# Kernel optimization log

Measured on AMD Instinct MI355X. Metric: run time of the kernel, lower is better.

The kernel has to match this reference:

```python
import math
import jax, jax.numpy as jnp
import numpy as np

HID = 256; NH = 8; DH = 32; DFF = 1024  # int(4.0*256)
N = 10000; E = 160000; NV = 128; NG = 64


def _ln(x, eps=1e-6):
    m = jnp.mean(x, axis=-1, keepdims=True)
    v = jnp.mean((x - m) ** 2, axis=-1, keepdims=True)
    return (x - m) * jax.lax.rsqrt(v + eps)


def _modulate(x, shift, scale):
    return x * (1.0 + scale) + shift


def _swiglu(x, W12, Wout):
    a, b = jnp.split(x @ W12, 2, axis=-1)
    return (jax.nn.silu(a) * b) @ Wout


def _adaln(t, W, b):
    return jnp.split(jax.nn.silu(t) @ W + b, 6, axis=-1)


def setup_inputs() -> dict:
    key = jax.random.key(0)
    ks = jax.random.split(key, 32)
    rn = lambda k, shape, s=1.0: jax.random.normal(k, shape, jnp.float32) * s
    W = 0.02
    return {
        "batch": jnp.sort(jax.random.randint(ks[0], (N,), 0, NG)),
        "x": rn(ks[1], (N, HID)),
        "t_emb_h": rn(ks[2], (N, HID)),
        "edge_attr": rn(ks[3], (E, HID)),
        "edge_index": jax.random.randint(ks[4], (2, E), 0, N),
        "t_emb_e": rn(ks[5], (E, HID)),
        "dist": rn(ks[6], (E, NV)),
        "W_edge_emb": rn(ks[7], (HID + NV, HID), W),
        "b_edge_emb": jnp.zeros((HID,), jnp.float32),
        "W_adaln": rn(ks[8], (HID, 6 * HID), W),
        "b_adaln": jnp.zeros((6 * HID,), jnp.float32),
        "W_adaln_e": rn(ks[9], (HID, 6 * HID), W),
        "b_adaln_e": jnp.zeros((6 * HID,), jnp.float32),
        "W_qkv": rn(ks[10], (HID, 3 * HID), W),
        "W_e0": rn(ks[11], (HID, HID), W),
        "W_e1": rn(ks[12], (HID, HID), W),
        "W_n2e": rn(ks[13], (HID, HID), W),
        "b_n2e": jnp.zeros((HID,), jnp.float32),
        "g_ln": jnp.ones((HID,), jnp.float32),
        "b_ln": jnp.zeros((HID,), jnp.float32),
        "W_ffn12": rn(ks[14], (HID, 2 * DFF), W),
        "W_ffn_out": rn(ks[15], (DFF, HID), W),
        "W_ffne12": rn(ks[16], (HID, 2 * DFF), W),
        "W_ffne_out": rn(ks[17], (DFF, HID), W),
    }


def reference(batch, x, t_emb_h, edge_attr, edge_index, t_emb_e, dist,
              W_edge_emb, b_edge_emb, W_adaln, b_adaln, W_adaln_e, b_adaln_e,
              W_qkv, W_e0, W_e1, W_n2e, b_n2e, g_ln, b_ln,
              W_ffn12, W_ffn_out, W_ffne12, W_ffne_out):
    src, tgt = edge_index[0], edge_index[1]
    n = x.shape[0]
    h_in_node = x
    h_in_edge = edge_attr

    shift_msa, scale_msa, gate_msa, shift_mlp, scale_mlp, gate_mlp = _adaln(t_emb_h, W_adaln, b_adaln)
    e_shift_msa, e_scale_msa, e_gate_msa, e_shift_mlp, e_scale_mlp, e_gate_mlp = _adaln(t_emb_e, W_adaln_e, b_adaln_e)

    edge_attr_e = jnp.concatenate([edge_attr, dist], axis=-1) @ W_edge_emb + b_edge_emb
    x_mod = _modulate(_ln(x), shift_msa, scale_msa)
    prev_edge_attr = edge_attr_e
    e_mod = _modulate(_ln(edge_attr_e), e_shift_msa, e_scale_msa)

    qkv = x_mod @ W_qkv                         # N x 3H
    Q, K, V = jnp.split(qkv, 3, axis=-1)
    Q = Q.reshape(-1, NH, DH)
    K = K.reshape(-1, NH, DH)
    V = V.reshape(-1, NH, DH)

    query_i = Q[src]                            # E x NH x DH
    key_j = K[tgt]
    value_j = V[tgt]
    edge_attn = jax.nn.gelu(e_mod @ W_e0, approximate=True).reshape(-1, NH, DH)

    alpha = jnp.sum(query_i * key_j * edge_attn, axis=-1) / math.sqrt(DH)  # E x NH
    # segment softmax over edges grouped by target node
    amax = jax.ops.segment_max(alpha, tgt, num_segments=n)                 # N x NH
    exp_a = jnp.exp(alpha - amax[tgt])
    denom = jax.ops.segment_sum(exp_a, tgt, num_segments=n)
    alpha = exp_a / denom[tgt]

    msg = value_j * (e_mod @ W_e1).reshape(-1, NH, DH) * alpha[..., None]
    out = jax.ops.segment_sum(msg.reshape(-1, NH * DH), tgt, num_segments=n)  # N x H

    h_node = out
    h_edge = (h_node[src] + h_node[tgt]) @ W_n2e + b_n2e

    h_node = h_in_node + gate_msa * h_node
    h_node = _modulate(_ln(h_node) * g_ln + b_ln, shift_mlp, scale_mlp)
    h_out = h_node + gate_mlp * _swiglu(h_node, W_ffn12, W_ffn_out)

    h_edge = h_in_edge + e_gate_msa * h_edge
    h_edge = _modulate(_ln(h_edge), e_shift_mlp, e_scale_mlp)
    h_edge_out = prev_edge_attr + h_edge + e_gate_mlp * _swiglu(h_edge, W_ffne12, W_ffne_out)
    return (h_out, h_edge_out)
```

## Files before the change

### kernel.cpp

```cpp
#include <hip/hip_runtime.h>

#define HID 256

typedef unsigned short u16;
typedef __attribute__((ext_vector_type(8))) short bf16x8;
typedef __attribute__((ext_vector_type(4))) float f32x4;

__device__ __forceinline__ float siluf(float x) { return x / (1.f + __expf(-x)); }
__device__ __forceinline__ float geluf(float x) {
    return x / (1.f + __expf(-(1.59576912f * x + 0.07135481f * x * x * x)));
}
__device__ __forceinline__ u16 f2b(float x) {
    unsigned u = __float_as_uint(x);
    unsigned r = u + 0x7FFFu + ((u >> 16) & 1u);
    return (u16)(r >> 16);
}
__device__ __forceinline__ float b2f(u16 h) {
    return __uint_as_float(((unsigned)h) << 16);
}
__device__ __forceinline__ void gload16(const u16* g, u16* l) {
    __builtin_amdgcn_global_load_lds(
        (const __attribute__((address_space(1))) unsigned int*)g,
        (__attribute__((address_space(3))) unsigned int*)l, 16, 0, 0);
}
__device__ __forceinline__ int imin(int a, int b) { return a < b ? a : b; }

__global__ __launch_bounds__(256) void gemm_mfma(
    const u16* __restrict__ A, int lda,
    const u16* __restrict__ Bt, int ldb,
    void* __restrict__ Cv, int ldc,
    int M, int N, int K,
    const float* __restrict__ bias, int act, int obf16)
{
    __shared__ u16 lds[8192];

    const int tid  = threadIdx.x;
    const int lane = tid & 63;
    const int wave = tid >> 6;
    const int row0 = blockIdx.y * 64;
    const int col0 = blockIdx.x * 128;
    const int wm   = (wave >> 1) * 32;
    const int wn   = (wave & 1) * 64;

    f32x4 acc[2][4];
#pragma unroll
    for (int i = 0; i < 2; ++i)
#pragma unroll
        for (int j = 0; j < 4; ++j) acc[i][j] = (f32x4)0.0f;

    const int kc = (lane & 3) * 8;
    const int rr  = wave * 16 + (lane >> 2);
    const int rb1 = (wave + 4) * 16 + (lane >> 2);
    const u16* pa  = A + (size_t)imin(row0 + rr, M - 1) * lda + kc;
    const u16* pb0 = Bt + (size_t)(col0 + rr) * ldb + kc;
    const u16* pb1 = Bt + (size_t)(col0 + rb1) * ldb + kc;
    u16* la  = &lds[wave * 512];
    u16* lb0 = &lds[2048 + wave * 512];
    u16* lb1 = &lds[2048 + (wave + 4) * 512];

    const int kb = (lane >> 4) * 8;
    const int fr = lane & 15;

    for (int k0 = 0; k0 < K; k0 += 32) {
        gload16(pa + k0, la);
        gload16(pb0 + k0, lb0);
        gload16(pb1 + k0, lb1);
        __syncthreads();

        bf16x8 af[2], bfm[4];
#pragma unroll
        for (int i = 0; i < 2; ++i)
            af[i] = *(const bf16x8*)&lds[(wm + i * 16 + fr) * 32 + kb];
#pragma unroll
        for (int j = 0; j < 4; ++j)
            bfm[j] = *(const bf16x8*)&lds[2048 + (wn + j * 16 + fr) * 32 + kb];
#pragma unroll
        for (int i = 0; i < 2; ++i)
#pragma unroll
            for (int j = 0; j < 4; ++j)
                acc[i][j] = __builtin_amdgcn_mfma_f32_16x16x32_bf16(af[i], bfm[j], acc[i][j], 0, 0, 0);
        __syncthreads();
    }

    const int qr = (lane >> 4) * 4;
    if (obf16) {
#pragma unroll
        for (int i = 0; i < 2; ++i)
#pragma unroll
            for (int r = 0; r < 4; ++r)
#pragma unroll
                for (int j = 0; j < 4; ++j) {
                    int lcol = wn + j * 16 + fr;
                    int gcol = col0 + lcol;
                    float v = acc[i][j][r];
                    if (bias) v += bias[gcol];
                    if (act == 2) v = geluf(v);
                    else if (act == 1) v = siluf(v);
                    else if (act == 4 && gcol < 256) v = geluf(v);
                    lds[(wm + i * 16 + qr + r) * 128 + lcol] = f2b(v);
                }
        __syncthreads();
        int row = tid >> 2, cc0 = (tid & 3) * 32;
        int grow = row0 + row;
        if (grow < M) {
            uint4* dst = (uint4*)((u16*)Cv + (size_t)grow * ldc + col0 + cc0);
            const uint4* sp = (const uint4*)&lds[row * 128 + cc0];
            dst[0] = sp[0]; dst[1] = sp[1]; dst[2] = sp[2]; dst[3] = sp[3];
        }
    } else {
        float* Cf = (float*)Cv;
#pragma unroll
        for (int i = 0; i < 2; ++i)
#pragma unroll
            for (int r = 0; r < 4; ++r) {
                int grow = row0 + wm + i * 16 + qr + r;
                if (grow >= M) continue;
#pragma unroll
                for (int j = 0; j < 4; ++j) {
                    int gcol = col0 + wn + j * 16 + fr;
                    float v = acc[i][j][r];
                    if (bias) v += bias[gcol];
                    if (act == 2) v = geluf(v);
                    else if (act == 1) v = siluf(v);
                    Cf[(size_t)grow * ldc + gcol] = v;
                }
            }
    }
}

__global__ __launch_bounds__(256) void gemm_ffn12(
    const u16* __restrict__ A, const u16* __restrict__ Wt,
    u16* __restrict__ C, int M)
{
    __shared__ u16 sm[6144];
    u16* lsA = sm;
    u16* lsB1 = sm + 2048;
    u16* lsB2 = sm + 4096;

    const int tid  = threadIdx.x;
    const int lane = tid & 63;
    const int wave = tid >> 6;
    const int row0 = blockIdx.y * 64;
    const int col0 = blockIdx.x * 64;
    const int wm   = (wave >> 1) * 32;
    const int wn   = (wave & 1) * 32;

    f32x4 accA[2][2], accB[2][2];
#pragma unroll
    for (int i = 0; i < 2; ++i)
#pragma unroll
        for (int j = 0; j < 2; ++j) { accA[i][j] = (f32x4)0.0f; accB[i][j] = (f32x4)0.0f; }

    const int kc = (lane & 3) * 8;
    const int rr = wave * 16 + (lane >> 2);
    const u16* pa  = A + (size_t)imin(row0 + rr, M - 1) * 256 + kc;
    const u16* pb1 = Wt + (size_t)(col0 + rr) * 256 + kc;
    const u16* pb2 = Wt + (size_t)(1024 + col0 + rr) * 256 + kc;
    u16* la  = &lsA[wave * 512];
    u16* lb1 = &lsB1[wave * 512];
    u16* lb2 = &lsB2[wave * 512];

    const int kb = (lane >> 4) * 8;
    const int fr = lane & 15;

#pragma unroll 1
    for (int k0 = 0; k0 < 256; k0 += 32) {
        gload16(pa + k0, la);
        gload16(pb1 + k0, lb1);
        gload16(pb2 + k0, lb2);
        __syncthreads();

        bf16x8 af[2], b1f[2], b2f_[2];
#pragma unroll
        for (int i = 0; i < 2; ++i)
            af[i] = *(const bf16x8*)&lsA[(wm + i * 16 + fr) * 32 + kb];
#pragma unroll
        for (int j = 0; j < 2; ++j) {
            b1f[j] = *(const bf16x8*)&lsB1[(wn + j * 16 + fr) * 32 + kb];
            b2f_[j] = *(const bf16x8*)&lsB2[(wn + j * 16 + fr) * 32 + kb];
        }
#pragma unroll
        for (int i = 0; i < 2; ++i)
#pragma unroll
            for (int j = 0; j < 2; ++j) {
                accA[i][j] = __builtin_amdgcn_mfma_f32_16x16x32_bf16(af[i], b1f[j], accA[i][j], 0, 0, 0);
                accB[i][j] = __builtin_amdgcn_mfma_f32_16x16x32_bf16(af[i], b2f_[j], accB[i][j], 0, 0, 0);
            }
        __syncthreads();
    }

    const int qr = (lane >> 4) * 4;
#pragma unroll
    for (int i = 0; i < 2; ++i)
#pragma unroll
        for (int r = 0; r < 4; ++r)
#pragma unroll
            for (int j = 0; j < 2; ++j) {
                float a = accA[i][j][r], b = accB[i][j][r];
                sm[(wm + i * 16 + qr + r) * 64 + wn + j * 16 + fr] = f2b(siluf(a) * b);
            }
    __syncthreads();
    int row = tid >> 2, cc0 = (tid & 3) * 16;
    int grow = row0 + row;
    if (grow < M) {
        uint4* dst = (uint4*)(C + (size_t)grow * 1024 + col0 + cc0);
        const uint4* sp = (const uint4*)&sm[row * 64 + cc0];
        dst[0] = sp[0]; dst[1] = sp[1];
    }
}

__global__ __launch_bounds__(256) void gemm_out_final(
    const u16* __restrict__ A, const u16* __restrict__ Bt,
    const float* __restrict__ eae, const u16* __restrict__ h2,
    const u16* __restrict__ gate, int ldg, int goff,
    float* __restrict__ out, int M)
{
    __shared__ u16 lds[6144];

    const int tid  = threadIdx.x;
    const int lane = tid & 63;
    const int wave = tid >> 6;
    const int row0 = blockIdx.y * 64;
    const int col0 = blockIdx.x * 128;
    const int wm   = (wave >> 1) * 32;
    const int wn   = (wave & 1) * 64;

    f32x4 acc[2][4];
#pragma unroll
    for (int i = 0; i < 2; ++i)
#pragma unroll
        for (int j = 0; j < 4; ++j) acc[i][j] = (f32x4)0.0f;

    const int kc = (lane & 3) * 8;
    const int rr = wave * 16 + (lane >> 2);
    const int rb0 = wave * 16 + (lane >> 2), rb1 = (wave + 4) * 16 + (lane >> 2);
    const u16* pa  = A + (size_t)imin(row0 + rr, M - 1) * 1024 + kc;
    const u16* pb0 = Bt + (size_t)(col0 + rb0) * 1024 + kc;
    const u16* pb1 = Bt + (size_t)(col0 + rb1) * 1024 + kc;
    u16* la  = &lds[wave * 512];
    u16* lb0 = &lds[2048 + wave * 512];
    u16* lb1 = &lds[2048 + (wave + 4) * 512];

    const int kb = (lane >> 4) * 8;
    const int fr = lane & 15;

#pragma unroll 1
    for (int k0 = 0; k0 < 1024; k0 += 32) {
        gload16(pa + k0, la);
        gload16(pb0 + k0, lb0);
        gload16(pb1 + k0, lb1);
        __syncthreads();

        bf16x8 af[2], bfm[4];
#pragma unroll
        for (int i = 0; i < 2; ++i)
            af[i] = *(const bf16x8*)&lds[(wm + i * 16 + fr) * 32 + kb];
#pragma unroll
        for (int j = 0; j < 4; ++j)
            bfm[j] = *(const bf16x8*)&lds[2048 + (wn + j * 16 + fr) * 32 + kb];
#pragma unroll
        for (int i = 0; i < 2; ++i)
#pragma unroll
            for (int j = 0; j < 4; ++j)
                acc[i][j] = __builtin_amdgcn_mfma_f32_16x16x32_bf16(af[i], bfm[j], acc[i][j], 0, 0, 0);
        __syncthreads();
    }

    const int qr = (lane >> 4) * 4;
#pragma unroll
    for (int i = 0; i < 2; ++i)
#pragma unroll
        for (int r = 0; r < 4; ++r) {
            int grow = row0 + wm + i * 16 + qr + r;
            if (grow >= M) continue;
#pragma unroll
            for (int j = 0; j < 4; ++j) {
                int gcol = col0 + wn + j * 16 + fr;
                size_t idx = (size_t)grow * 256 + gcol;
                float v = acc[i][j][r] * b2f(gate[(size_t)grow * ldg + goff + gcol]) + b2f(h2[idx]);
                if (eae) v += eae[idx];
                out[idx] = v;
            }
        }
}

__global__ __launch_bounds__(256) void k_wconv(
    const float* __restrict__ W, u16* __restrict__ Wt, int K, int N)
{
    int i = blockIdx.x * 256 + threadIdx.x;
    if (i >= K * N) return;
    int n = i / K, k = i - n * K;
    Wt[i] = f2b(W[(size_t)k * N + n]);
}

__global__ __launch_bounds__(256) void k_silu_b16(
    const float* __restrict__ src, u16* __restrict__ dst, long long n4)
{
    long long i = (long long)blockIdx.x * 256 + threadIdx.x;
    if (i >= n4) return;
    float4 v = ((const float4*)src)[i];
    ushort4 o;
    o.x = f2b(siluf(v.x)); o.y = f2b(siluf(v.y)); o.z = f2b(siluf(v.z)); o.w = f2b(siluf(v.w));
    ((ushort4*)dst)[i] = o;
}

__global__ __launch_bounds__(256) void k_pack_ed(
    const float* __restrict__ ea_, const float* __restrict__ dist,
    u16* __restrict__ out, long long cnt4)
{
    long long i = (long long)blockIdx.x * 256 + threadIdx.x;
    if (i >= cnt4) return;
    long long r = i / 96;
    int c4 = (int)(i - r * 96) * 4;
    float4 v = (c4 < 256) ? *(const float4*)(ea_ + r * 256 + c4)
                          : *(const float4*)(dist + r * 128 + (c4 - 256));
    ushort4 o;
    o.x = f2b(v.x); o.y = f2b(v.y); o.z = f2b(v.z); o.w = f2b(v.w);
    *(ushort4*)(out + r * 384 + c4) = o;
}

__global__ __launch_bounds__(256) void k_ln_mod_b16(
    const float* __restrict__ X, u16* __restrict__ Y, int M,
    const u16* __restrict__ ssb, int ldss, int shoff, int scoff)
{
    int row = (blockIdx.x << 2) + (threadIdx.x >> 6);
    if (row >= M) return;
    int lane = threadIdx.x & 63;
    const float* xr = X + (size_t)row * HID + lane * 4;
    float x0 = xr[0], x1 = xr[1], x2 = xr[2], x3 = xr[3];
    float s = x0 + x1 + x2 + x3;
    float q = x0 * x0 + x1 * x1 + x2 * x2 + x3 * x3;
#pragma unroll
    for (int o = 32; o; o >>= 1) { s += __shfl_xor(s, o, 64); q += __shfl_xor(q, o, 64); }
    float m = s * (1.f / HID);
    float r = rsqrtf(q * (1.f / HID) - m * m + 1e-6f);
    const u16* sp = ssb + (size_t)row * ldss;
    ushort4 sh = *(const ushort4*)(sp + shoff + lane * 4);
    ushort4 sc = *(const ushort4*)(sp + scoff + lane * 4);
    ushort4 o;
    o.x = f2b((x0 - m) * r * (1.f + b2f(sc.x)) + b2f(sh.x));
    o.y = f2b((x1 - m) * r * (1.f + b2f(sc.y)) + b2f(sh.y));
    o.z = f2b((x2 - m) * r * (1.f + b2f(sc.z)) + b2f(sh.z));
    o.w = f2b((x3 - m) * r * (1.f + b2f(sc.w)) + b2f(sh.w));
    ((ushort4*)(Y + (size_t)row * HID))[lane] = o;
}

__global__ __launch_bounds__(256) void k_ln_mod_resid_b16(
    const float* __restrict__ A, const float* __restrict__ Bv, u16* __restrict__ Y, int M,
    const u16* __restrict__ gb, int ldg, int goff,
    const u16* __restrict__ ssb, int ldss, int shoff, int scoff,
    const float* __restrict__ gw, const float* __restrict__ bw)
{
    int row = (blockIdx.x << 2) + (threadIdx.x >> 6);
    if (row >= M) return;
    int lane = threadIdx.x & 63;
    const float* ar = A + (size_t)row * HID + lane * 4;
    const float* br = Bv + (size_t)row * HID + lane * 4;
    ushort4 gp = *(const ushort4*)(gb + (size_t)row * ldg + goff + lane * 4);
    float t0 = ar[0] + b2f(gp.x) * br[0];
    float t1 = ar[1] + b2f(gp.y) * br[1];
    float t2 = ar[2] + b2f(gp.z) * br[2];
    float t3 = ar[3] + b2f(gp.w) * br[3];
    float s = t0 + t1 + t2 + t3;
    float q = t0 * t0 + t1 * t1 + t2 * t2 + t3 * t3;
#pragma unroll
    for (int o = 32; o; o >>= 1) { s += __shfl_xor(s, o, 64); q += __shfl_xor(q, o, 64); }
    float m = s * (1.f / HID);
    float r = rsqrtf(q * (1.f / HID) - m * m + 1e-6f);
    float n0 = (t0 - m) * r, n1 = (t1 - m) * r, n2 = (t2 - m) * r, n3 = (t3 - m) * r;
    if (gw) {
        const float* g4 = gw + lane * 4;
        const float* b4 = bw + lane * 4;
        n0 = n0 * g4[0] + b4[0]; n1 = n1 * g4[1] + b4[1];
        n2 = n2 * g4[2] + b4[2]; n3 = n3 * g4[3] + b4[3];
    }
    const u16* sp = ssb + (size_t)row * ldss;
    ushort4 sh = *(const ushort4*)(sp + shoff + lane * 4);
    ushort4 sc = *(const ushort4*)(sp + scoff + lane * 4);
    ushort4 o;
    o.x = f2b(n0 * (1.f + b2f(sc.x)) + b2f(sh.x));
    o.y = f2b(n1 * (1.f + b2f(sc.y)) + b2f(sh.y));
    o.z = f2b(n2 * (1.f + b2f(sc.z)) + b2f(sh.z));
    o.w = f2b(n3 * (1.f + b2f(sc.w)) + b2f(sh.w));
    ((ushort4*)(Y + (size_t)row * HID))[lane] = o;
}

__global__ __launch_bounds__(256) void attn_alpha_k(
    const u16* __restrict__ qkv, const u16* __restrict__ ea, int lde,
    const int* __restrict__ src, const int* __restrict__ tgt,
    float* __restrict__ alpha)
{
    int e = blockIdx.x;
    int t = threadIdx.x;
    int h = t >> 5, d = t & 31;
    int s = src[e], g = tgt[e];
    float qv = b2f(qkv[(size_t)s * 768 + h * 32 + d]);
    float kv = b2f(qkv[(size_t)g * 768 + 256 + h * 32 + d]);
    float wv = b2f(ea[(size_t)e * lde + t]);
    float v = qv * kv * wv;
#pragma unroll
    for (int o = 16; o; o >>= 1) v += __shfl_xor(v, o, 32);
    if (d == 0) alpha[(size_t)e * 8 + h] = v * 0.17677669529663687f;
}

__global__ __launch_bounds__(256) void k_hist(
    const int* __restrict__ tgt, int* __restrict__ counts, int E)
{
    int i = blockIdx.x * 256 + threadIdx.x;
    if (i < E) atomicAdd(&counts[tgt[i]], 1);
}

__global__ __launch_bounds__(256) void k_scan(
    const int* __restrict__ counts, int* __restrict__ offsets, int Nn)
{
    __shared__ int part[256];
    __shared__ int pref[257];
    int t = threadIdx.x;
    int chunk = (Nn + 255) / 256;
    int lo = t * chunk, hi = imin(lo + chunk, Nn);
    int s = 0;
    for (int i = lo; i < hi; ++i) s += counts[i];
    part[t] = s;
    __syncthreads();
    if (t == 0) {
        int run = 0;
        for (int i = 0; i < 256; ++i) { pref[i] = run; run += part[i]; }
        pref[256] = run;
        offsets[Nn] = run;
    }
    __syncthreads();
    int run = pref[t];
    for (int i = lo; i < hi; ++i) { offsets[i] = run; run += counts[i]; }
}

__global__ __launch_bounds__(256) void k_scatter(
    const int* __restrict__ tgt, int* __restrict__ cursor,
    int* __restrict__ eidlist, int E)
{
    int i = blockIdx.x * 256 + threadIdx.x;
    if (i < E) {
        int pos = atomicAdd(&cursor[tgt[i]], 1);
        eidlist[pos] = i;
    }
}

__global__ __launch_bounds__(256) void k_amax_den(
    const float* __restrict__ alpha, const int* __restrict__ offsets,
    const int* __restrict__ eidlist, float* __restrict__ amaxF,
    float* __restrict__ invden, int NH8)
{
    int i = blockIdx.x * 256 + threadIdx.x;
    if (i >= NH8) return;
    int n = i >> 3, h = i & 7;
    int b = offsets[n], e = offsets[n + 1];
    float m = -1e30f;
    for (int k = b; k < e; ++k) m = fmaxf(m, alpha[(size_t)eidlist[k] * 8 + h]);
    float s = 0.f;
    for (int k = b; k < e; ++k) s += __expf(alpha[(size_t)eidlist[k] * 8 + h] - m);
    amaxF[i] = m;
    invden[i] = (s > 0.f) ? 1.f / s : 0.f;
}

__global__ __launch_bounds__(256) void k_norm(
    float* __restrict__ alpha, const float* __restrict__ amaxF,
    const float* __restrict__ invden, const int* __restrict__ tgt, int EH)
{
    int i = blockIdx.x * 256 + threadIdx.x;
    if (i >= EH) return;
    int e = i >> 3, h = i & 7;
    int g = tgt[e];
    alpha[i] = __expf(alpha[i] - amaxF[(size_t)g * 8 + h]) * invden[(size_t)g * 8 + h];
}

__global__ __launch_bounds__(256) void attn_msg_csr(
    const u16* __restrict__ qkv, const u16* __restrict__ ea1,
    const float* __restrict__ alpha, const int* __restrict__ offsets,
    const int* __restrict__ eidlist, float* __restrict__ hattn)
{
    int n = blockIdx.x;
    int c = threadIdx.x;
    int h = c >> 5;
    int b = offsets[n], e = offsets[n + 1];
    float acc = 0.f;
    for (int k = b; k < e; ++k) {
        int eid = eidlist[k];
        float w = alpha[(size_t)eid * 8 + h];
        acc += b2f(ea1[(size_t)eid * 512 + 256 + c]) * w;
    }
    hattn[(size_t)n * 256 + c] = b2f(qkv[(size_t)n * 768 + 512 + c]) * acc;
}

__global__ __launch_bounds__(256) void k_gsum_b16(
    const float* __restrict__ hattn, const int* __restrict__ src, const int* __restrict__ tgt,
    u16* __restrict__ g, long long cnt4)
{
    long long i = (long long)blockIdx.x * 256 + threadIdx.x;
    if (i >= cnt4) return;
    long long e = i >> 6;
    int c4 = (int)(i & 63) * 4;
    float4 a = *(const float4*)(hattn + (size_t)src[e] * 256 + c4);
    float4 b = *(const float4*)(hattn + (size_t)tgt[e] * 256 + c4);
    ushort4 o;
    o.x = f2b(a.x + b.x); o.y = f2b(a.y + b.y); o.z = f2b(a.z + b.z); o.w = f2b(a.w + b.w);
    ((ushort4*)g)[i] = o;
}

static inline void gemm(hipStream_t st, const u16* A, int lda, const u16* Bt, int ldb,
                        void* C, int ldc, int M, int N, int K,
                        const float* bias, int act, int obf16)
{
    dim3 g(N / 128, (M + 63) / 64);
    hipLaunchKernelGGL(gemm_mfma, g, dim3(256), 0, st, A, lda, Bt, ldb, C, ldc, M, N, K,
                       bias, act, obf16);
}

extern "C" void kernel_launch(void* const* d_in, const int* in_sizes, int n_in,
                              void* d_out, int out_size, void* d_ws, size_t ws_size,
                              hipStream_t stream)
{
    const int Nn = in_sizes[0];
    const int E = in_sizes[3] / HID;

    const float* x        = (const float*)d_in[1];
    const float* t_emb_h  = (const float*)d_in[2];
    const float* edge_attr= (const float*)d_in[3];
    const int*   eidx     = (const int*)d_in[4];
    const float* t_emb_e  = (const float*)d_in[5];
    const float* dist     = (const float*)d_in[6];
    const float* W_ee     = (const float*)d_in[7];
    const float* b_ee     = (const float*)d_in[8];
    const float* W_ad     = (const float*)d_in[9];
    const float* b_ad     = (const float*)d_in[10];
    const float* W_ade    = (const float*)d_in[11];
    const float* b_ade    = (const float*)d_in[12];
    const float* W_qkv    = (const float*)d_in[13];
    const float* W_e0     = (const float*)d_in[14];
    const float* W_e1     = (const float*)d_in[15];
    const float* W_n2e    = (const float*)d_in[16];
    const float* b_n2e    = (const float*)d_in[17];
    const float* g_ln     = (const float*)d_in[18];
    const float* b_ln     = (const float*)d_in[19];
    const float* W_f12    = (const float*)d_in[20];
    const float* W_fout   = (const float*)d_in[21];
    const float* W_fe12   = (const float*)d_in[22];
    const float* W_feout  = (const float*)d_in[23];

    const int* src = eidx;
    const int* tgt = eidx + E;

    float* outN = (float*)d_out;
    float* outE = (float*)d_out + (size_t)Nn * 256;

    char* W = (char*)d_ws;
    size_t off = 0;
    auto alloc = [&](size_t bytes) -> size_t {
        size_t o = off; off += (bytes + 255) & ~(size_t)255; return o;
    };
    float*    alpha = (float*)(W + alloc((size_t)E * 8 * 4));
    float*    amaxF = (float*)(W + alloc((size_t)Nn * 8 * 4));
    float*    invden= (float*)(W + alloc((size_t)Nn * 8 * 4));
    float*    hat   = (float*)(W + alloc((size_t)Nn * 256 * 4));
    int*      offs  = (int*)(W + alloc((size_t)(Nn + 1) * 4));
    int*      cursor= (int*)(W + alloc((size_t)Nn * 4));
    int*      eidl  = (int*)(W + alloc((size_t)E * 4));
    u16*      qkvb  = (u16*)(W + alloc((size_t)Nn * 768 * 2));
    u16*      sth   = (u16*)(W + alloc((size_t)Nn * 256 * 2));
    u16*      steb  = (u16*)(W + alloc((size_t)E * 256 * 2));
    u16*      ea1b  = (u16*)(W + alloc((size_t)E * 512 * 2));
    u16*      adnb  = (u16*)(W + alloc((size_t)Nn * 1536 * 2));
    u16*      xmb   = (u16*)(W + alloc((size_t)Nn * 256 * 2));
    u16*      h2nb  = (u16*)(W + alloc((size_t)Nn * 256 * 2));
    u16*      cnb   = (u16*)(W + alloc((size_t)Nn * 1024 * 2));
    u16* weet   = (u16*)(W + alloc((size_t)256 * 384 * 2));
    u16* wadt   = (u16*)(W + alloc((size_t)1536 * 256 * 2));
    u16* wadet  = (u16*)(W + alloc((size_t)1536 * 256 * 2));
    u16* wqkvt  = (u16*)(W + alloc((size_t)768 * 256 * 2));
    u16* we01t  = (u16*)(W + alloc((size_t)512 * 256 * 2));
    u16* wn2et  = (u16*)(W + alloc((size_t)256 * 256 * 2));
    u16* wf12t  = (u16*)(W + alloc((size_t)2048 * 256 * 2));
    u16* wfoutt = (u16*)(W + alloc((size_t)256 * 1024 * 2));
    u16* wfe12t = (u16*)(W + alloc((size_t)2048 * 256 * 2));
    u16* wfeoutt= (u16*)(W + alloc((size_t)256 * 1024 * 2));

    char* pool = W + off;
    size_t poolB = (ws_size > off) ? (ws_size - off) : 0;
    auto chunkRowsB = [&](size_t bytesPerRow, int total) -> int {
        long c = (long)(poolB / bytesPerRow);
        c = (c / 256) * 256;
        if (c < 256) c = 256;
        if (c > total) c = (long)total;
        return (int)c;
    };

    hipMemsetAsync(cursor, 0, (size_t)Nn * 4, stream);
    hipLaunchKernelGGL(k_hist, dim3((E + 255) / 256), dim3(256), 0, stream, tgt, cursor, E);
    hipLaunchKernelGGL(k_scan, dim3(1), dim3(256), 0, stream, cursor, offs, Nn);
    hipMemcpyAsync(cursor, offs, (size_t)Nn * 4, hipMemcpyDeviceToDevice, stream);
    hipLaunchKernelGGL(k_scatter, dim3((E + 255) / 256), dim3(256), 0, stream,
                       tgt, cursor, eidl, E);

    {
        struct WC { const float* w; u16* wt; int K, N; } wl[] = {
            { W_ee,    weet,   384, 256 },
            { W_ad,    wadt,   256, 1536 },
            { W_ade,   wadet,  256, 1536 },
            { W_qkv,   wqkvt,  256, 768 },
            { W_e0,    we01t,  256, 256 },
            { W_e1,    we01t + 256 * 256, 256, 256 },
            { W_n2e,   wn2et,  256, 256 },
            { W_f12,   wf12t,  256, 2048 },
            { W_fout,  wfoutt, 1024, 256 },
            { W_fe12,  wfe12t, 256, 2048 },
            { W_feout, wfeoutt,1024, 256 },
        };
        for (auto& e : wl) {
            int cnt = e.K * e.N;
            hipLaunchKernelGGL(k_wconv, dim3((cnt + 255) / 256), dim3(256), 0, stream,
                               e.w, e.wt, e.K, e.N);
        }
    }

    hipLaunchKernelGGL(k_silu_b16, dim3((unsigned)(((long long)Nn * 64 + 255) / 256)), dim3(256),
                       0, stream, t_emb_h, sth, (long long)Nn * 64);
    hipLaunchKernelGGL(k_silu_b16, dim3((unsigned)(((long long)E * 64 + 255) / 256)), dim3(256),
                       0, stream, t_emb_e, steb, (long long)E * 64);

    gemm(stream, sth, 256, wadt, 256, adnb, 1536, Nn, 1536, 256, b_ad, 0, 1);
    hipLaunchKernelGGL(k_ln_mod_b16, dim3((Nn + 3) / 4), dim3(256), 0, stream,
                       x, xmb, Nn, adnb, 1536, 0, 256);
    gemm(stream, xmb, 256, wqkvt, 256, qkvb, 768, Nn, 768, 256, nullptr, 0, 1);

    {
        int C = chunkRowsB(1536 + 1024 + 512, E);
        char* p = pool;
        u16* eab2 = (u16*)p; p += (size_t)C * 1536;
        u16* emsb = (u16*)p; p += (size_t)C * 1024;
        u16* emod = (u16*)p;
        for (int s = 0; s < E; s += C) {
            int cc = (E - s < C) ? (E - s) : C;
            float* eaeC = outE + (size_t)s * 256;
            hipLaunchKernelGGL(k_pack_ed, dim3((unsigned)(((long long)cc * 96 + 255) / 256)),
                               dim3(256), 0, stream, edge_attr + (size_t)s * 256,
                               dist + (size_t)s * 128, eab2, (long long)cc * 96);
            gemm(stream, eab2, 384, weet, 384, eaeC, 256, cc, 256, 384, b_ee, 0, 0);
            gemm(stream, steb + (size_t)s * 256, 256, wadet, 256, emsb, 512, cc, 512, 256,
                 b_ade, 0, 1);
            hipLaunchKernelGGL(k_ln_mod_b16, dim3((cc + 3) / 4), dim3(256), 0, stream,
                               eaeC, emod, cc, emsb, 512, 0, 256);
            gemm(stream, emod, 256, we01t, 256, ea1b + (size_t)s * 512, 512, cc, 512, 256,
                 nullptr, 4, 1);
            hipLaunchKernelGGL(attn_alpha_k, dim3(cc), dim3(256), 0, stream,
                               qkvb, ea1b + (size_t)s * 512, 512, src + s, tgt + s,
                               alpha + (size_t)s * 8);
        }
    }

    hipLaunchKernelGGL(k_amax_den, dim3((Nn * 8 + 255) / 256), dim3(256), 0, stream,
                       alpha, offs, eidl, amaxF, invden, Nn * 8);
    hipLaunchKernelGGL(k_norm, dim3((E * 8 + 255) / 256), dim3(256), 0, stream,
                       alpha, amaxF, invden, tgt, E * 8);

    hipLaunchKernelGGL(attn_msg_csr, dim3(Nn), dim3(256), 0, stream,
                       qkvb, ea1b, alpha, offs, eidl, hat);

    hipLaunchKernelGGL(k_ln_mod_resid_b16, dim3((Nn + 3) / 4), dim3(256), 0, stream,
                       x, hat, h2nb, Nn, adnb, 1536, 512, adnb, 1536, 768, 1024, g_ln, b_ln);
    hipLaunchKernelGGL(gemm_ffn12, dim3(16, (Nn + 63) / 64), dim3(256), 0, stream,
                       h2nb, wf12t, cnb, Nn);
    hipLaunchKernelGGL(gemm_out_final, dim3(2, (Nn + 63) / 64), dim3(256), 0, stream,
                       cnb, wfoutt, (const float*)nullptr, h2nb, adnb, 1536, 1280, outN, Nn);

    {
        int C = chunkRowsB(512 + 2048 + 1024 + 512 + 2048, E);
        char* p = pool;
        u16*   gsum = (u16*)p;  p += (size_t)C * 512;
        u16*   em2b = (u16*)p;  p += (size_t)C * 2048;
        float* hep  = (float*)p; p += (size_t)C * 1024;
        u16*   h2e  = (u16*)p;  p += (size_t)C * 512;
        u16*   cne  = (u16*)p;
        for (int s = 0; s < E; s += C) {
            int cc = (E - s < C) ? (E - s) : C;
            hipLaunchKernelGGL(k_gsum_b16, dim3((unsigned)(((long long)cc * 64 + 255) / 256)),
                               dim3(256), 0, stream, hat, src + s, tgt + s, gsum, (long long)cc * 64);
            gemm(stream, gsum, 256, wn2et, 256, hep, 256, cc, 256, 256, b_n2e, 0, 0);
            gemm(stream, steb + (size_t)s * 256, 256, wadet + 512 * 256, 256, em2b, 1024,
                 cc, 1024, 256, b_ade + 512, 0, 1);
            hipLaunchKernelGGL(k_ln_mod_resid_b16, dim3((cc + 3) / 4), dim3(256), 0, stream,
                               edge_attr + (size_t)s * 256, hep, h2e, cc,
                               em2b, 1024, 0, em2b, 1024, 256, 512, nullptr, nullptr);
            hipLaunchKernelGGL(gemm_ffn12, dim3(16, (cc + 63) / 64), dim3(256), 0, stream,
                               h2e, wfe12t, cne, cc);
            hipLaunchKernelGGL(gemm_out_final, dim3(2, (cc + 63) / 64), dim3(256), 0, stream,
                               cne, wfeoutt, outE + (size_t)s * 256, h2e,
                               em2b, 1024, 768, outE + (size_t)s * 256, cc);
        }
    }
    (void)n_in; (void)out_size;
}
```

Baseline: 2.234 ms.

## Double-buffer LDS tiles in MFMA GEMM kernels to overlap loads with compute

Converts the generic GEMM, the fused SwiGLU ffn12 GEMM and the final output GEMM from single-buffered LDS staging to ping-pong double buffering. The next K-slice is issued with global_load_lds into the alternate buffer before the MFMAs on the current buffer run, and each iteration keeps one barrier instead of two. The goal is to hide global-load latency behind matrix math. In exchange, LDS per block doubles (up to 24 KB), which can reduce occupancy, and an extra barrier is added before the epilogues that reuse LDS.

```diff
diff --git a/kernel.cpp b/kernel.cpp
--- a/kernel.cpp
+++ b/kernel.cpp
@@ -32,7 +32,7 @@
     int M, int N, int K,
     const float* __restrict__ bias, int act, int obf16)
 {
-    __shared__ u16 lds[8192];
+    __shared__ u16 lds[12288];
 
     const int tid  = threadIdx.x;
     const int lane = tid & 63;
@@ -54,36 +54,42 @@
     const u16* pa  = A + (size_t)imin(row0 + rr, M - 1) * lda + kc;
     const u16* pb0 = Bt + (size_t)(col0 + rr) * ldb + kc;
     const u16* pb1 = Bt + (size_t)(col0 + rb1) * ldb + kc;
-    u16* la  = &lds[wave * 512];
-    u16* lb0 = &lds[2048 + wave * 512];
-    u16* lb1 = &lds[2048 + (wave + 4) * 512];
 
     const int kb = (lane >> 4) * 8;
     const int fr = lane & 15;
 
+    auto stage = [&](int buf, int k0) {
+        u16* base = &lds[buf * 6144];
+        gload16(pa + k0, base + wave * 512);
+        gload16(pb0 + k0, base + 2048 + wave * 512);
+        gload16(pb1 + k0, base + 2048 + (wave + 4) * 512);
+    };
+
+    stage(0, 0);
+    __syncthreads();
+    int cur = 0;
     for (int k0 = 0; k0 < K; k0 += 32) {
-        gload16(pa + k0, la);
-        gload16(pb0 + k0, lb0);
-        gload16(pb1 + k0, lb1);
-        __syncthreads();
-
+        bool more = (k0 + 32 < K);
+        if (more) stage(cur ^ 1, k0 + 32);
+        const u16* base = &lds[cur * 6144];
         bf16x8 af[2], bfm[4];
 #pragma unroll
         for (int i = 0; i < 2; ++i)
-            af[i] = *(const bf16x8*)&lds[(wm + i * 16 + fr) * 32 + kb];
+            af[i] = *(const bf16x8*)&base[(wm + i * 16 + fr) * 32 + kb];
 #pragma unroll
         for (int j = 0; j < 4; ++j)
-            bfm[j] = *(const bf16x8*)&lds[2048 + (wn + j * 16 + fr) * 32 + kb];
+            bfm[j] = *(const bf16x8*)&base[2048 + (wn + j * 16 + fr) * 32 + kb];
 #pragma unroll
         for (int i = 0; i < 2; ++i)
 #pragma unroll
             for (int j = 0; j < 4; ++j)
                 acc[i][j] = __builtin_amdgcn_mfma_f32_16x16x32_bf16(af[i], bfm[j], acc[i][j], 0, 0, 0);
-        __syncthreads();
+        if (more) { __syncthreads(); cur ^= 1; }
     }
 
     const int qr = (lane >> 4) * 4;
     if (obf16) {
+        __syncthreads();
 #pragma unroll
         for (int i = 0; i < 2; ++i)
 #pragma unroll
@@ -132,10 +138,7 @@
     const u16* __restrict__ A, const u16* __restrict__ Wt,
     u16* __restrict__ C, int M)
 {
-    __shared__ u16 sm[6144];
-    u16* lsA = sm;
-    u16* lsB1 = sm + 2048;
-    u16* lsB2 = sm + 4096;
+    __shared__ u16 sm[12288];
 
     const int tid  = threadIdx.x;
     const int lane = tid & 63;
@@ -156,28 +159,33 @@
     const u16* pa  = A + (size_t)imin(row0 + rr, M - 1) * 256 + kc;
     const u16* pb1 = Wt + (size_t)(col0 + rr) * 256 + kc;
     const u16* pb2 = Wt + (size_t)(1024 + col0 + rr) * 256 + kc;
-    u16* la  = &lsA[wave * 512];
-    u16* lb1 = &lsB1[wave * 512];
-    u16* lb2 = &lsB2[wave * 512];
 
     const int kb = (lane >> 4) * 8;
     const int fr = lane & 15;
 
+    auto stage = [&](int buf, int k0) {
+        u16* base = &sm[buf * 6144];
+        gload16(pa + k0, base + wave * 512);
+        gload16(pb1 + k0, base + 2048 + wave * 512);
+        gload16(pb2 + k0, base + 4096 + wave * 512);
+    };
+
+    stage(0, 0);
+    __syncthreads();
+    int cur = 0;
 #pragma unroll 1
     for (int k0 = 0; k0 < 256; k0 += 32) {
-        gload16(pa + k0, la);
-        gload16(pb1 + k0, lb1);
-        gload16(pb2 + k0, lb2);
-        __syncthreads();
-
+        bool more = (k0 + 32 < 256);
+        if (more) stage(cur ^ 1, k0 + 32);
+        const u16* base = &sm[cur * 6144];
         bf16x8 af[2], b1f[2], b2f_[2];
 #pragma unroll
         for (int i = 0; i < 2; ++i)
-            af[i] = *(const bf16x8*)&lsA[(wm + i * 16 + fr) * 32 + kb];
+            af[i] = *(const bf16x8*)&base[(wm + i * 16 + fr) * 32 + kb];
 #pragma unroll
         for (int j = 0; j < 2; ++j) {
-            b1f[j] = *(const bf16x8*)&lsB1[(wn + j * 16 + fr) * 32 + kb];
-            b2f_[j] = *(const bf16x8*)&lsB2[(wn + j * 16 + fr) * 32 + kb];
+            b1f[j] = *(const bf16x8*)&base[2048 + (wn + j * 16 + fr) * 32 + kb];
+            b2f_[j] = *(const bf16x8*)&base[4096 + (wn + j * 16 + fr) * 32 + kb];
         }
 #pragma unroll
         for (int i = 0; i < 2; ++i)
@@ -186,10 +194,11 @@
                 accA[i][j] = __builtin_amdgcn_mfma_f32_16x16x32_bf16(af[i], b1f[j], accA[i][j], 0, 0, 0);
                 accB[i][j] = __builtin_amdgcn_mfma_f32_16x16x32_bf16(af[i], b2f_[j], accB[i][j], 0, 0, 0);
             }
-        __syncthreads();
+        if (more) { __syncthreads(); cur ^= 1; }
     }
 
     const int qr = (lane >> 4) * 4;
+    __syncthreads();
 #pragma unroll
     for (int i = 0; i < 2; ++i)
 #pragma unroll
@@ -215,7 +224,7 @@
     const u16* __restrict__ gate, int ldg, int goff,
     float* __restrict__ out, int M)
 {
-    __shared__ u16 lds[6144];
+    __shared__ u16 lds[12288];
 
     const int tid  = threadIdx.x;
     const int lane = tid & 63;
@@ -233,37 +242,42 @@
 
     const int kc = (lane & 3) * 8;
     const int rr = wave * 16 + (lane >> 2);
-    const int rb0 = wave * 16 + (lane >> 2), rb1 = (wave + 4) * 16 + (lane >> 2);
+    const int rb1 = (wave + 4) * 16 + (lane >> 2);
     const u16* pa  = A + (size_t)imin(row0 + rr, M - 1) * 1024 + kc;
-    const u16* pb0 = Bt + (size_t)(col0 + rb0) * 1024 + kc;
+    const u16* pb0 = Bt + (size_t)(col0 + rr) * 1024 + kc;
     const u16* pb1 = Bt + (size_t)(col0 + rb1) * 1024 + kc;
-    u16* la  = &lds[wave * 512];
-    u16* lb0 = &lds[2048 + wave * 512];
-    u16* lb1 = &lds[2048 + (wave + 4) * 512];
 
     const int kb = (lane >> 4) * 8;
     const int fr = lane & 15;
 
+    auto stage = [&](int buf, int k0) {
+        u16* base = &lds[buf * 6144];
+        gload16(pa + k0, base + wave * 512);
+        gload16(pb0 + k0, base + 2048 + wave * 512);
+        gload16(pb1 + k0, base + 2048 + (wave + 4) * 512);
+    };
+
+    stage(0, 0);
+    __syncthreads();
+    int cur = 0;
 #pragma unroll 1
     for (int k0 = 0; k0 < 1024; k0 += 32) {
-        gload16(pa + k0, la);
-        gload16(pb0 + k0, lb0);
-        gload16(pb1 + k0, lb1);
-        __syncthreads();
-
+        bool more = (k0 + 32 < 1024);
+        if (more) stage(cur ^ 1, k0 + 32);
+        const u16* base = &lds[cur * 6144];
         bf16x8 af[2], bfm[4];
 #pragma unroll
         for (int i = 0; i < 2; ++i)
-            af[i] = *(const bf16x8*)&lds[(wm + i * 16 + fr) * 32 + kb];
+            af[i] = *(const bf16x8*)&base[(wm + i * 16 + fr) * 32 + kb];
 #pragma unroll
         for (int j = 0; j < 4; ++j)
-            bfm[j] = *(const bf16x8*)&lds[2048 + (wn + j * 16 + fr) * 32 + kb];
+            bfm[j] = *(const bf16x8*)&base[2048 + (wn + j * 16 + fr) * 32 + kb];
 #pragma unroll
         for (int i = 0; i < 2; ++i)
 #pragma unroll
             for (int j = 0; j < 4; ++j)
                 acc[i][j] = __builtin_amdgcn_mfma_f32_16x16x32_bf16(af[i], bfm[j], acc[i][j], 0, 0, 0);
-        __syncthreads();
+        if (more) { __syncthreads(); cur ^= 1; }
     }
 
     const int qr = (lane >> 4) * 4;
```

After: 2.344 ms. 4.9% more time.
